# Kernel tuning notes

Hardware: AMD Instinct MI355X
Metric: run time of the kernel (lower is better)

The kernel has to match this reference:

```python
import jax, jax.numpy as jnp
import numpy as np

# pywt db2 decomposition filters
DEC_LO = np.array([-0.12940952255092145, 0.22414386804185735,
                   0.8365163037378079, 0.4829629131445341], dtype=np.float32)
DEC_HI = np.array([-0.4829629131445341, 0.8365163037378079,
                   -0.22414386804185735, -0.12940952255092145], dtype=np.float32)
LEVEL = 3
REC_WEIGHT = 1.0
FILT_LEN = 4
PAD = (2 * FILT_LEN - 3) // 2  # = 2, ptwt reflect padding per side


def _filters(dtype):
    # ptwt uses cross-correlation with flipped pywt filters (== true convolution)
    lo = jnp.asarray(DEC_LO[::-1].copy(), dtype=dtype)
    hi = jnp.asarray(DEC_HI[::-1].copy(), dtype=dtype)
    ll = jnp.outer(lo, lo)  # 'a'
    lh = jnp.outer(hi, lo)  # 'h'
    hl = jnp.outer(lo, hi)  # 'v'
    hh = jnp.outer(hi, hi)  # 'd'
    return jnp.stack([ll, lh, hl, hh])[:, None]  # [4,1,4,4]


def _dwt_step(x, filt):
    # x: [N, nb, H, W] -> [N, 4*nb, H', W'] (each band split into a,h,v,d; grouped)
    n, nb, h, w = x.shape
    padb = PAD + (h % 2)
    padr = PAD + (w % 2)
    xp = jnp.pad(x, ((0, 0), (0, 0), (PAD, padb), (PAD, padr)), mode='reflect')
    k = jnp.tile(filt, (nb, 1, 1, 1))  # [4*nb, 1, 4, 4]
    return jax.lax.conv_general_dilated(
        xp, k, window_strides=(2, 2), padding='VALID',
        feature_group_count=nb,
        dimension_numbers=('NCHW', 'OIHW', 'NCHW'))


def setup_inputs() -> dict:
    key = jax.random.key(0)
    k1, k2 = jax.random.split(key)
    preds = jax.random.normal(k1, (64, 3, 512, 512), dtype=jnp.float32)
    targets = jax.random.normal(k2, (64, 3, 512, 512), dtype=jnp.float32)
    return {"preds": preds, "targets": targets}


def reference(preds, targets):
    n, c, h, w = preds.shape
    p = preds.reshape(n * c, 1, h, w)
    t = targets.reshape(n * c, 1, h, w)
    filt = _filters(preds.dtype)
    for _ in range(LEVEL):
        p = _dwt_step(p, filt)
        t = _dwt_step(t, filt)
    # p, t: [N*C, 4**LEVEL, h', w']; leaf 0 is the all-'a' (pure approx) packet
    per_leaf_mse = jnp.mean((p - t) ** 2, axis=(0, 2, 3))  # [4**LEVEL]
    wvec = jnp.ones(per_leaf_mse.shape[0], dtype=preds.dtype).at[0].set(0.5)
    return REC_WEIGHT * jnp.dot(wvec, per_leaf_mse)
```

## Files before the change

### kernel.cpp

```cpp
#include <hip/hip_runtime.h>

#define F_LO0 0.4829629131445341f
#define F_LO1 0.8365163037378079f
#define F_LO2 0.22414386804185735f
#define F_LO3 (-0.12940952255092145f)
#define F_HI0 (-0.12940952255092145f)
#define F_HI1 (-0.22414386804185735f)
#define F_HI2 0.8365163037378079f
#define F_HI3 (-0.4829629131445341f)

__device__ __forceinline__ int reflect_idx(int r, int n) {
    r = (r < 0) ? -r : r;
    r = (r >= n) ? 2 * n - 2 - r : r;
    return r;
}

__device__ __forceinline__ float4 vfilt(const float4 a, const float4 b,
                                        const float4 c, const float4 d,
                                        float c0, float c1, float c2, float c3) {
    return make_float4(c0 * a.x + c1 * b.x + c2 * c.x + c3 * d.x,
                       c0 * a.y + c1 * b.y + c2 * c.y + c3 * d.y,
                       c0 * a.z + c1 * b.z + c2 * c.z + c3 * d.z,
                       c0 * a.w + c1 * b.w + c2 * c.w + c3 * d.w);
}

__device__ __forceinline__ void hfilt2(const float4 x0, const float4 x1, const float4 x2,
                                       float4& lo, float4& hi) {
    lo.x = F_LO0 * x0.z + F_LO1 * x0.w + F_LO2 * x1.x + F_LO3 * x1.y;
    lo.y = F_LO0 * x1.x + F_LO1 * x1.y + F_LO2 * x1.z + F_LO3 * x1.w;
    lo.z = F_LO0 * x1.z + F_LO1 * x1.w + F_LO2 * x2.x + F_LO3 * x2.y;
    lo.w = F_LO0 * x2.x + F_LO1 * x2.y + F_LO2 * x2.z + F_LO3 * x2.w;
    hi.x = F_HI0 * x0.z + F_HI1 * x0.w + F_HI2 * x1.x + F_HI3 * x1.y;
    hi.y = F_HI0 * x1.x + F_HI1 * x1.y + F_HI2 * x1.z + F_HI3 * x1.w;
    hi.z = F_HI0 * x1.z + F_HI1 * x1.w + F_HI2 * x2.x + F_HI3 * x2.y;
    hi.w = F_HI0 * x2.x + F_HI1 * x2.y + F_HI2 * x2.z + F_HI3 * x2.w;
}

__global__ void __launch_bounds__(512, 6) k_wpt_fused(
    const float* __restrict__ p, const float* __restrict__ t,
    float* __restrict__ partial) {
    constexpr int N0 = 512, N1 = 257, N2 = 130, N3 = 66;

    __shared__ __align__(16) float sA[6240];
    __shared__ __align__(16) float sB[6912];
    __shared__ float wsum[8];

    int bid = blockIdx.x;
    int swz = (bid & 7) * (int)(gridDim.x >> 3) + (bid >> 3);
    int img = swz / 81;
    int tt = swz - img * 81;
    int TA = (tt / 9) * 8;
    int TB = (tt % 9) * 8;

    const int tid = threadIdx.x;
    const size_t ibase = (size_t)img * (N0 * N0);

    const int O0r = 8 * TA - 14, O0c = 8 * TB - 16;
    const int O1r = 4 * TA - 6, O1c = 4 * TB - 6;
    const int O2r = 2 * TA - 2, O2c = 2 * TB - 2;
    const bool edge = (TA == 0) || (TA == 64) || (TB == 0) || (TB == 64);

    if (!edge) {
        const float* __restrict__ pb = p + ibase + (size_t)O0r * N0 + O0c;
        const float* __restrict__ tb = t + ibase + (size_t)O0r * N0 + O0c;
#pragma unroll
        for (int it = 0; it < 4; ++it) {
            int e = it * 512 + tid;
            if (e < 1560) {
                int r = e / 20, q = e - r * 20;
                const float4 pv = *(const float4*)(pb + (size_t)r * N0 + 4 * q);
                const float4 tv = *(const float4*)(tb + (size_t)r * N0 + 4 * q);
                *(float4*)(sA + r * 80 + ((q ^ (r & 1)) << 2)) =
                    make_float4(pv.x - tv.x, pv.y - tv.y, pv.z - tv.z, pv.w - tv.w);
            }
        }
    } else {
#pragma unroll
        for (int it = 0; it < 4; ++it) {
            int e = it * 512 + tid;
            if (e < 1560) {
                int r = e / 20, q = e - r * 20;
                int gr = reflect_idx(O0r + r, N0);
                const float* pr = p + ibase + (size_t)gr * N0;
                const float* tr = t + ibase + (size_t)gr * N0;
                float v[4];
#pragma unroll
                for (int x = 0; x < 4; ++x) {
                    int gc = reflect_idx(O0c + 4 * q + x, N0);
                    v[x] = pr[gc] - tr[gc];
                }
                *(float4*)(sA + r * 80 + ((q ^ (r & 1)) << 2)) =
                    make_float4(v[0], v[1], v[2], v[3]);
            }
        }
    }
    __syncthreads();

#pragma unroll
    for (int it = 0; it < 2; ++it) {
        int e = it * 512 + tid;
        if (e < 780) {
            int r = e / 10, k = e - r * 10;
            int r1 = r & 1;
            const float* row = sA + r * 80;
            int q2 = 2 * k + 2; if (q2 > 19) q2 = 18;
            float4 x0 = *(const float4*)(row + (((2 * k) ^ r1) << 2));
            float4 x1 = *(const float4*)(row + (((2 * k + 1) ^ r1) << 2));
            float4 x2 = *(const float4*)(row + ((q2 ^ r1) << 2));
            float4 lo, hi;
            hfilt2(x0, x1, x2, lo, hi);
            *(float4*)(sB + r * 40 + 4 * k) = lo;
            *(float4*)(sB + 3120 + r * 40 + 4 * k) = hi;
        }
    }
    __syncthreads();

    if (tid < 380) {
        int r1 = tid / 10, k = tid - r1 * 10;
        const float* blo = sB + (2 * r1) * 40 + 4 * k;
        const float* bhi = blo + 3120;
        float4 L0 = *(const float4*)(blo);
        float4 L1v = *(const float4*)(blo + 40);
        float4 L2v = *(const float4*)(blo + 80);
        float4 L3v = *(const float4*)(blo + 120);
        float4 H0 = *(const float4*)(bhi);
        float4 H1 = *(const float4*)(bhi + 40);
        float4 H2 = *(const float4*)(bhi + 80);
        float4 H3 = *(const float4*)(bhi + 120);
        float4 b0 = vfilt(L0, L1v, L2v, L3v, F_LO0, F_LO1, F_LO2, F_LO3);
        float4 b1 = vfilt(L0, L1v, L2v, L3v, F_HI0, F_HI1, F_HI2, F_HI3);
        float4 b2 = vfilt(H0, H1, H2, H3, F_LO0, F_LO1, F_LO2, F_LO3);
        float4 b3 = vfilt(H0, H1, H2, H3, F_HI0, F_HI1, F_HI2, F_HI3);
        int wo = r1 * 40 + 4 * k;
        *(float4*)(sA + wo) = b0;
        *(float4*)(sA + 1520 + wo) = b1;
        *(float4*)(sA + 3040 + wo) = b2;
        *(float4*)(sA + 4560 + wo) = b3;
    }
    __syncthreads();
    if (edge) {
#pragma unroll
        for (int it = 0; it < 3; ++it) {
            int e = it * 512 + tid;
            if (e < 1444) {
                int lr = e / 38, lc = e - lr * 38;
                int sr = reflect_idx(O1r + lr, N1) - O1r;
                int sc = reflect_idx(O1c + lc, N1) - O1c;
                if ((sr != lr || sc != lc) && (unsigned)sr < 38u && (unsigned)sc < 38u) {
                    int da = lr * 40 + lc;
                    int sa = sr * 40 + sc;
                    sA[da] = sA[sa];
                    sA[1520 + da] = sA[1520 + sa];
                    sA[3040 + da] = sA[3040 + sa];
                    sA[4560 + da] = sA[4560 + sa];
                }
            }
        }
        __syncthreads();
    }

    const int w = tid >> 6;
    const int ln = tid & 63;
    const int bnd = w >> 1;
    const int hf = w & 1;
    const int off = hf * 6;
    float* scr = sB + w * 864;
    const float* L1b = sA + bnd * 1520;

    if (ln < 54) {
        const int c = ln % 18, s = ln / 18;
#pragma unroll
        for (int tq = 0; tq < 4; ++tq) {
            const int r2l = 3 * tq + s;
            const float* base = L1b + (2 * (off + r2l)) * 40 + 2 * c;
            float lo[4], hi[4];
#pragma unroll
            for (int u = 0; u < 4; ++u) {
                float2 a = *(const float2*)(base + u * 40);
                float2 d = *(const float2*)(base + u * 40 + 2);
                lo[u] = F_LO0 * a.x + F_LO1 * a.y + F_LO2 * d.x + F_LO3 * d.y;
                hi[u] = F_HI0 * a.x + F_HI1 * a.y + F_HI2 * d.x + F_HI3 * d.y;
            }
            int sl = r2l * 18 + c;
            scr[sl]       = F_LO0 * lo[0] + F_LO1 * lo[1] + F_LO2 * lo[2] + F_LO3 * lo[3];
            scr[sl + 216] = F_HI0 * lo[0] + F_HI1 * lo[1] + F_HI2 * lo[2] + F_HI3 * lo[3];
            scr[sl + 432] = F_LO0 * hi[0] + F_LO1 * hi[1] + F_LO2 * hi[2] + F_LO3 * hi[3];
            scr[sl + 648] = F_HI0 * hi[0] + F_HI1 * hi[1] + F_HI2 * hi[2] + F_HI3 * hi[3];
        }
    }

    if (edge) {
#pragma unroll
        for (int q = 0; q < 4; ++q) {
            int e = q * 54 + ln;
            if (ln < 54 && e < 216) {
                int lr = e / 18, lc = e - lr * 18;
                int srt = reflect_idx(O2r + off + lr, N2) - O2r - off;
                int sct = reflect_idx(O2c + lc, N2) - O2c;
                if ((srt != lr || sct != lc) &&
                    (unsigned)srt < 12u && (unsigned)sct < 18u) {
                    int d = lr * 18 + lc, sidx = srt * 18 + sct;
#pragma unroll
                    for (int pl = 0; pl < 4; ++pl)
                        scr[d + 216 * pl] = scr[sidx + 216 * pl];
                }
            }
        }
    }

    float local = 0.f;
    {
        const int pp = ln >> 5, rem = ln & 31, r3 = rem >> 3, j = rem & 7;
        const int i = hf * 4 + r3;
        const int sr0 = 2 * r3 + hf * 2;
        const bool valid = (TA + i < N3) && (TB + j < N3);
#pragma unroll
        for (int pi = 0; pi < 2; ++pi) {
            const int pl = 2 * pp + pi;
            const float* pb = scr + pl * 216 + sr0 * 18 + 2 * j;
            float lo[4], hi[4];
#pragma unroll
            for (int u = 0; u < 4; ++u) {
                float2 a = *(const float2*)(pb + u * 18);
                float2 d = *(const float2*)(pb + u * 18 + 2);
                lo[u] = F_LO0 * a.x + F_LO1 * a.y + F_LO2 * d.x + F_LO3 * d.y;
                hi[u] = F_HI0 * a.x + F_HI1 * a.y + F_HI2 * d.x + F_HI3 * d.y;
            }
            float o0 = F_LO0 * lo[0] + F_LO1 * lo[1] + F_LO2 * lo[2] + F_LO3 * lo[3];
            float o1 = F_HI0 * lo[0] + F_HI1 * lo[1] + F_HI2 * lo[2] + F_HI3 * lo[3];
            float o2 = F_LO0 * hi[0] + F_LO1 * hi[1] + F_LO2 * hi[2] + F_LO3 * hi[3];
            float o3 = F_HI0 * hi[0] + F_HI1 * hi[1] + F_HI2 * hi[2] + F_HI3 * hi[3];
            if (valid) {
                float w00 = (bnd == 0 && pl == 0) ? 0.5f : 1.0f;
                local += w00 * o0 * o0 + o1 * o1 + o2 * o2 + o3 * o3;
            }
        }
    }

#pragma unroll
    for (int o = 32; o > 0; o >>= 1) local += __shfl_down(local, o, 64);
    if (ln == 0) wsum[w] = local;
    __syncthreads();
    if (tid == 0) {
        float ssum = 0.f;
#pragma unroll
        for (int x = 0; x < 8; ++x) ssum += wsum[x];
        partial[blockIdx.x] = ssum;
    }
}

__global__ void __launch_bounds__(1024) k_reduce(const float* __restrict__ part,
                                                 float* __restrict__ out,
                                                 int n4, float inv_den) {
    const int tid = threadIdx.x;
    float s = 0.f;
    const float4* p4 = (const float4*)part;
    for (int i = tid; i < n4; i += 1024) {
        float4 v = p4[i];
        s += v.x + v.y + v.z + v.w;
    }
#pragma unroll
    for (int o = 32; o > 0; o >>= 1) s += __shfl_down(s, o, 64);
    __shared__ float ws_[16];
    int w = tid >> 6;
    if ((tid & 63) == 0) ws_[w] = s;
    __syncthreads();
    if (tid == 0) {
        float tot = 0.f;
#pragma unroll
        for (int i = 0; i < 16; ++i) tot += ws_[i];
        out[0] = tot * inv_den;
    }
}

extern "C" void kernel_launch(void* const* d_in, const int* in_sizes, int n_in,
                              void* d_out, int out_size, void* d_ws, size_t ws_size,
                              hipStream_t stream) {
    const float* preds = (const float*)d_in[0];
    const float* targets = (const float*)d_in[1];
    float* out = (float*)d_out;
    float* partial = (float*)d_ws;

    const float inv_den = 1.0f / (192.0f * 66.0f * 66.0f);
    const int nblk = 192 * 9 * 9;

    k_wpt_fused<<<dim3(nblk), dim3(512), 0, stream>>>(preds, targets, partial);
    k_reduce<<<dim3(1), dim3(1024), 0, stream>>>(partial, out, nblk / 4, inv_den);
}
```

Measured before the change: 207.0 us.

## Fuse global load with level-1 horizontal filter, bypassing shared staging

Each of 390 threads now loads a 20-wide row segment of preds and targets straight into registers, forms the difference, and runs the level-1 horizontal low/high filter there before writing to sB. This removes the sA staging pass and one __syncthreads, and keeps the reflect-padding path only for segments near the image boundary. In exchange, fewer threads issue global loads (390 rather than 512), each thread holds more registers, and the per-thread loads are strided 64 bytes apart so coalescing is weaker than before.

```diff
diff --git a/kernel.cpp b/kernel.cpp
--- a/kernel.cpp
+++ b/kernel.cpp
@@ -24,24 +24,12 @@
                        c0 * a.w + c1 * b.w + c2 * c.w + c3 * d.w);
 }
 
-__device__ __forceinline__ void hfilt2(const float4 x0, const float4 x1, const float4 x2,
-                                       float4& lo, float4& hi) {
-    lo.x = F_LO0 * x0.z + F_LO1 * x0.w + F_LO2 * x1.x + F_LO3 * x1.y;
-    lo.y = F_LO0 * x1.x + F_LO1 * x1.y + F_LO2 * x1.z + F_LO3 * x1.w;
-    lo.z = F_LO0 * x1.z + F_LO1 * x1.w + F_LO2 * x2.x + F_LO3 * x2.y;
-    lo.w = F_LO0 * x2.x + F_LO1 * x2.y + F_LO2 * x2.z + F_LO3 * x2.w;
-    hi.x = F_HI0 * x0.z + F_HI1 * x0.w + F_HI2 * x1.x + F_HI3 * x1.y;
-    hi.y = F_HI0 * x1.x + F_HI1 * x1.y + F_HI2 * x1.z + F_HI3 * x1.w;
-    hi.z = F_HI0 * x1.z + F_HI1 * x1.w + F_HI2 * x2.x + F_HI3 * x2.y;
-    hi.w = F_HI0 * x2.x + F_HI1 * x2.y + F_HI2 * x2.z + F_HI3 * x2.w;
-}
-
 __global__ void __launch_bounds__(512, 6) k_wpt_fused(
     const float* __restrict__ p, const float* __restrict__ t,
     float* __restrict__ partial) {
     constexpr int N0 = 512, N1 = 257, N2 = 130, N3 = 66;
 
-    __shared__ __align__(16) float sA[6240];
+    __shared__ __align__(16) float sA[6080];
     __shared__ __align__(16) float sB[6912];
     __shared__ float wsum[8];
 
@@ -60,58 +48,53 @@
     const int O2r = 2 * TA - 2, O2c = 2 * TB - 2;
     const bool edge = (TA == 0) || (TA == 64) || (TB == 0) || (TB == 64);
 
-    if (!edge) {
-        const float* __restrict__ pb = p + ibase + (size_t)O0r * N0 + O0c;
-        const float* __restrict__ tb = t + ibase + (size_t)O0r * N0 + O0c;
-#pragma unroll
-        for (int it = 0; it < 4; ++it) {
-            int e = it * 512 + tid;
-            if (e < 1560) {
-                int r = e / 20, q = e - r * 20;
-                const float4 pv = *(const float4*)(pb + (size_t)r * N0 + 4 * q);
-                const float4 tv = *(const float4*)(tb + (size_t)r * N0 + 4 * q);
-                *(float4*)(sA + r * 80 + ((q ^ (r & 1)) << 2)) =
-                    make_float4(pv.x - tv.x, pv.y - tv.y, pv.z - tv.z, pv.w - tv.w);
-            }
-        }
-    } else {
-#pragma unroll
-        for (int it = 0; it < 4; ++it) {
-            int e = it * 512 + tid;
-            if (e < 1560) {
-                int r = e / 20, q = e - r * 20;
-                int gr = reflect_idx(O0r + r, N0);
-                const float* pr = p + ibase + (size_t)gr * N0;
-                const float* tr = t + ibase + (size_t)gr * N0;
-                float v[4];
-#pragma unroll
-                for (int x = 0; x < 4; ++x) {
-                    int gc = reflect_idx(O0c + 4 * q + x, N0);
-                    v[x] = pr[gc] - tr[gc];
-                }
-                *(float4*)(sA + r * 80 + ((q ^ (r & 1)) << 2)) =
-                    make_float4(v[0], v[1], v[2], v[3]);
-            }
-        }
-    }
-    __syncthreads();
-
-#pragma unroll
-    for (int it = 0; it < 2; ++it) {
-        int e = it * 512 + tid;
-        if (e < 780) {
-            int r = e / 10, k = e - r * 10;
-            int r1 = r & 1;
-            const float* row = sA + r * 80;
-            int q2 = 2 * k + 2; if (q2 > 19) q2 = 18;
-            float4 x0 = *(const float4*)(row + (((2 * k) ^ r1) << 2));
-            float4 x1 = *(const float4*)(row + (((2 * k + 1) ^ r1) << 2));
-            float4 x2 = *(const float4*)(row + ((q2 ^ r1) << 2));
-            float4 lo, hi;
-            hfilt2(x0, x1, x2, lo, hi);
-            *(float4*)(sB + r * 40 + 4 * k) = lo;
-            *(float4*)(sB + 3120 + r * 40 + 4 * k) = hi;
-        }
+    if (tid < 390) {
+        unsigned ru = (unsigned)tid / 5u;
+        const int r = (int)ru;
+        const int k = tid - (int)(5u * ru);
+        const int grr = reflect_idx(O0r + r, N0);
+        const float* __restrict__ prow = p + ibase + (size_t)grr * N0;
+        const float* __restrict__ trow = t + ibase + (size_t)grr * N0;
+        const int gc0 = O0c + 16 * k;
+        float v[20];
+        if ((unsigned)gc0 <= 492u) {
+#pragma unroll
+            for (int q = 0; q < 5; ++q) {
+                const float4 pv = *(const float4*)(prow + gc0 + 4 * q);
+                const float4 tv = *(const float4*)(trow + gc0 + 4 * q);
+                v[4 * q + 0] = pv.x - tv.x;
+                v[4 * q + 1] = pv.y - tv.y;
+                v[4 * q + 2] = pv.z - tv.z;
+                v[4 * q + 3] = pv.w - tv.w;
+            }
+        } else {
+#pragma unroll
+            for (int x = 0; x < 20; ++x) {
+                int gc = reflect_idx(gc0 + x, N0);
+                v[x] = prow[gc] - trow[gc];
+            }
+        }
+        float* dst = sB + r * 40 + 8 * k;
+        *(float4*)(dst) = make_float4(
+            F_LO0 * v[2] + F_LO1 * v[3] + F_LO2 * v[4] + F_LO3 * v[5],
+            F_LO0 * v[4] + F_LO1 * v[5] + F_LO2 * v[6] + F_LO3 * v[7],
+            F_LO0 * v[6] + F_LO1 * v[7] + F_LO2 * v[8] + F_LO3 * v[9],
+            F_LO0 * v[8] + F_LO1 * v[9] + F_LO2 * v[10] + F_LO3 * v[11]);
+        *(float4*)(dst + 4) = make_float4(
+            F_LO0 * v[10] + F_LO1 * v[11] + F_LO2 * v[12] + F_LO3 * v[13],
+            F_LO0 * v[12] + F_LO1 * v[13] + F_LO2 * v[14] + F_LO3 * v[15],
+            F_LO0 * v[14] + F_LO1 * v[15] + F_LO2 * v[16] + F_LO3 * v[17],
+            F_LO0 * v[16] + F_LO1 * v[17] + F_LO2 * v[18] + F_LO3 * v[19]);
+        *(float4*)(dst + 3120) = make_float4(
+            F_HI0 * v[2] + F_HI1 * v[3] + F_HI2 * v[4] + F_HI3 * v[5],
+            F_HI0 * v[4] + F_HI1 * v[5] + F_HI2 * v[6] + F_HI3 * v[7],
+            F_HI0 * v[6] + F_HI1 * v[7] + F_HI2 * v[8] + F_HI3 * v[9],
+            F_HI0 * v[8] + F_HI1 * v[9] + F_HI2 * v[10] + F_HI3 * v[11]);
+        *(float4*)(dst + 3124) = make_float4(
+            F_HI0 * v[10] + F_HI1 * v[11] + F_HI2 * v[12] + F_HI3 * v[13],
+            F_HI0 * v[12] + F_HI1 * v[13] + F_HI2 * v[14] + F_HI3 * v[15],
+            F_HI0 * v[14] + F_HI1 * v[15] + F_HI2 * v[16] + F_HI3 * v[17],
+            F_HI0 * v[16] + F_HI1 * v[17] + F_HI2 * v[18] + F_HI3 * v[19]);
     }
     __syncthreads();
 
```

After: 205.2 us. No clear change (-0.9%).
